# Kernel optimization log

Hardware: AMD Instinct MI355X
Metric: run time of the kernel (lower is better)

Reference implementation:

```python
import jax, jax.numpy as jnp
import numpy as np

B, N, D = 8, 1024, 256
H = 8
DH = D // H
R = 4          # relation types 0..3; adj value 4 = no relation
FF = 1024
EPS = 1e-5


def _lin(k, fan_in, shape):
    return jax.random.normal(k, shape, jnp.float32) * (1.0 / np.sqrt(fan_in))


def setup_inputs() -> dict:
    key = jax.random.key(0)
    ks = jax.random.split(key, 16)
    src = jax.random.normal(ks[0], (B, N, D), jnp.float32)
    adj_matrix = jax.random.randint(ks[1], (B, N, N), 0, 5, dtype=jnp.int32)
    Wq = _lin(ks[2], D, (D, D)); bq = jnp.zeros((D,), jnp.float32)
    Wk = _lin(ks[3], D, (D, D)); bk = jnp.zeros((D,), jnp.float32)
    Wv = _lin(ks[4], D, (R, D, D)); bv = jnp.zeros((R, D), jnp.float32)
    Wo = _lin(ks[5], D, (D, D)); bo = jnp.zeros((D,), jnp.float32)
    W1 = _lin(ks[6], D, (D, FF)); b1 = jnp.zeros((FF,), jnp.float32)
    W2 = _lin(ks[7], FF, (FF, D)); b2 = jnp.zeros((D,), jnp.float32)
    g1 = jnp.ones((D,), jnp.float32); beta1 = jnp.zeros((D,), jnp.float32)
    g2 = jnp.ones((D,), jnp.float32); beta2 = jnp.zeros((D,), jnp.float32)
    return dict(src=src, adj_matrix=adj_matrix, Wq=Wq, bq=bq, Wk=Wk, bk=bk,
                Wv=Wv, bv=bv, Wo=Wo, bo=bo, W1=W1, b1=b1, W2=W2, b2=b2,
                g1=g1, beta1=beta1, g2=g2, beta2=beta2)


def _ln(x, g, b):
    m = x.mean(-1, keepdims=True)
    v = ((x - m) ** 2).mean(-1, keepdims=True)
    return (x - m) * jax.lax.rsqrt(v + EPS) * g + b


def reference(src, adj_matrix, Wq, bq, Wk, bk, Wv, bv, Wo, bo, W1, b1, W2, b2, g1, beta1, g2, beta2):
    Bb, Nn, Dm = src.shape
    h, dh = H, Dm // H
    q = (src @ Wq + bq).reshape(Bb, Nn, h, dh).transpose(0, 2, 1, 3)  # (B,H,N,dh)
    k = (src @ Wk + bk).reshape(Bb, Nn, h, dh).transpose(0, 2, 1, 3)
    scores = jnp.einsum('bhid,bhjd->bhij', q, k) / np.sqrt(dh)
    attn = jax.nn.softmax(scores, axis=-1)                             # (B,H,N,N)
    out = jnp.zeros_like(q)
    for r in range(Wv.shape[0]):  # small fixed relation loop, matches module
        v_r = (src @ Wv[r] + bv[r]).reshape(Bb, Nn, h, dh).transpose(0, 2, 1, 3)
        mask = (adj_matrix == r)[:, None]                              # (B,1,N,N)
        out = out + jnp.einsum('bhij,bhjd->bhid', attn * mask, v_r)
    attn_out = out.transpose(0, 2, 1, 3).reshape(Bb, Nn, Dm) @ Wo + bo
    x = _ln(src + attn_out, g1, beta1)
    ff = jax.nn.gelu(x @ W1 + b1, approximate=False) @ W2 + b2
    return _ln(x + ff, g2, beta2)
```

## Files before the change

kernel.cpp:

```cpp
#include <hip/hip_runtime.h>
#include <hip/hip_bf16.h>
#include <cmath>

constexpr int CB  = 8;
constexpr int CN  = 1024;
constexpr int CD  = 256;
constexpr int CH  = 8;
constexpr int CDH = 32;
constexpr int CR  = 4;
constexpr int CFF = 1024;
constexpr float CEPS = 1e-5f;
constexpr float CS = 0.25503480f;
constexpr size_t SZH = (size_t)CB * CH * CN * CDH;

#define MODE_QK    0
#define MODE_FFN1  2
#define MODE_VT    4

typedef float v4f __attribute__((ext_vector_type(4)));
typedef short v8s __attribute__((ext_vector_type(8)));

static __device__ __forceinline__ short f2bf(float f) {
    unsigned u = __builtin_bit_cast(unsigned, f);
    u += 0x7fff + ((u >> 16) & 1);
    return (short)(u >> 16);
}
static __device__ __forceinline__ float bf2f(short s) {
    unsigned u = ((unsigned)(unsigned short)s) << 16;
    return __builtin_bit_cast(float, u);
}
static __device__ __forceinline__ unsigned cvtpk_bf16(float lo, float hi) {
    unsigned r;
    asm("v_cvt_pk_bf16_f32 %0, %1, %2" : "=v"(r) : "v"(lo), "v"(hi));
    return r;
}

static __device__ __forceinline__ void async_copy16(const void* g, void* l) {
    __builtin_amdgcn_global_load_lds(
        (const __attribute__((address_space(1))) void*)g,
        (__attribute__((address_space(3))) void*)l, 16, 0, 0);
}

template<int BM, int BN, int MODE>
__device__ __forceinline__ void gemm_body(
    const short* __restrict__ A, const short* __restrict__ Bw,
    const float* __restrict__ biasv, void* __restrict__ dest,
    int M, int K, int Nw, int bx, int by, short* smem)
{
    constexpr int WTM = BM / 2, WTN = BN / 2;
    constexpr int TM = WTM / 16, TN = WTN / 16;
    short* As = smem;
    short* Bs = smem + 2 * BM * 32;

    const int t    = threadIdx.x;
    const int lane = t & 63;
    const int w    = t >> 6;
    const int quad = lane >> 4, l15 = lane & 15;
    const int wm = w >> 1, wn = w & 1;
    const int m0 = bx * BM, n0 = by * BN;

    const int srow = lane >> 2;
    const int scol = (lane & 3) * 8;

    v4f acc[TM][TN];
    #pragma unroll
    for (int i = 0; i < TM; ++i)
        #pragma unroll
        for (int j = 0; j < TN; ++j) acc[i][j] = (v4f){0.f, 0.f, 0.f, 0.f};

    const int NK = K >> 5;

    auto stage = [&](int buf, int kt) {
        #pragma unroll
        for (int u = 0; u < BM / 64; ++u) {
            const int e0 = (w * (BM / 64) + u) * 512;
            const int row = (e0 >> 5) + srow;
            async_copy16(A + (size_t)(m0 + row) * K + kt + scol,
                         &As[buf * BM * 32 + e0]);
        }
        #pragma unroll
        for (int u = 0; u < BN / 64; ++u) {
            const int e0 = (w * (BN / 64) + u) * 512;
            const int row = (e0 >> 5) + srow;
            async_copy16(Bw + (size_t)(n0 + row) * K + kt + scol,
                         &Bs[buf * BN * 32 + e0]);
        }
    };

    stage(0, 0);

    for (int it = 0; it < NK; ++it) {
        __syncthreads();
        if (it + 1 < NK) stage((it + 1) & 1, (it + 1) << 5);

        const int buf = it & 1;
        v8s af[TM], bfr[TN];
        #pragma unroll
        for (int i = 0; i < TM; ++i)
            af[i] = *(const v8s*)&As[buf * BM * 32 +
                                     (wm * WTM + i * 16 + l15) * 32 + quad * 8];
        #pragma unroll
        for (int j = 0; j < TN; ++j)
            bfr[j] = *(const v8s*)&Bs[buf * BN * 32 +
                                      (wn * WTN + j * 16 + l15) * 32 + quad * 8];
        #pragma unroll
        for (int i = 0; i < TM; ++i)
            #pragma unroll
            for (int j = 0; j < TN; ++j)
                acc[i][j] = __builtin_amdgcn_mfma_f32_16x16x32_bf16(
                    af[i], bfr[j], acc[i][j], 0, 0, 0);
    }

    #pragma unroll
    for (int i = 0; i < TM; ++i) {
        #pragma unroll
        for (int j = 0; j < TN; ++j) {
            const int mb = m0 + wm * WTM + i * 16 + quad * 4;
            const int n  = n0 + wn * WTN + j * 16 + l15;
            float vals[4];
            if (MODE == MODE_VT) {
                #pragma unroll
                for (int rr = 0; rr < 4; ++rr) vals[rr] = acc[i][j][rr] + biasv[mb + rr];
            } else {
                #pragma unroll
                for (int rr = 0; rr < 4; ++rr) vals[rr] = acc[i][j][rr] + biasv[n];
            }

            if (MODE == MODE_QK) {
                if (n0 < 256) {
                    #pragma unroll
                    for (int rr = 0; rr < 4; ++rr) vals[rr] *= CS;
                }
                const int b = mb >> 10, ii0 = mb & 1023;
                const int plane = n >> 8, nn = n & 255;
                const int h = nn >> 5, d = nn & 31;
                #pragma unroll
                for (int rr = 0; rr < 4; ++rr)
                    ((short*)dest)[(size_t)plane * SZH +
                        (((size_t)(b * CH + h)) * CN + ii0 + rr) * CDH + d] =
                        f2bf(vals[rr]);
            } else if (MODE == MODE_VT) {
                const int b = n >> 10, ii = n & 1023;
                const int iip = (ii & ~63) | ((ii & 15) << 2) | ((ii >> 4) & 3);
                #pragma unroll
                for (int rr = 0; rr < 4; ++rr) {
                    const int m = mb + rr;
                    const int r2 = m >> 8, hd = m & 255;
                    const int h = hd >> 5, d = hd & 31;
                    ((short*)dest)[2 * SZH +
                        (((size_t)(r2 * 64 + b * CH + h)) * CDH + d) * CN + iip] =
                        f2bf(vals[rr]);
                }
            } else {
                #pragma unroll
                for (int rr = 0; rr < 4; ++rr) {
                    const size_t idx = (size_t)(mb + rr) * Nw + n;
                    const float xx = vals[rr];
                    const float E = exp2f(2.302217f * (xx + 0.044715f * xx * xx * xx));
                    ((short*)dest)[idx] = f2bf(xx * E / (E + 1.f));
                }
            }
        }
    }
}

template<int BM, int BN, int MODE>
__global__ __launch_bounds__(256)
void gemm_mfma(const short* __restrict__ A, const short* __restrict__ Bw,
               const float* __restrict__ biasv, void* __restrict__ dest,
               int M, int K, int Nw)
{
    extern __shared__ short smem[];
    gemm_body<BM, BN, MODE>(A, Bw, biasv, dest, M, K, Nw,
                            blockIdx.x, blockIdx.y, smem);
}

__global__ __launch_bounds__(256)
void proj_kernel(const short* __restrict__ src_bf, const short* __restrict__ wqkvT,
                 const float* __restrict__ bpack, short* __restrict__ qkv,
                 const int* __restrict__ adj, unsigned char* __restrict__ adj4)
{
    extern __shared__ short smem[];
    const int g = blockIdx.x;
    if (g < 512) {
        gemm_body<64, 128, MODE_QK>(src_bf, wqkvT, bpack, qkv,
                                    8192, 256, 512, g >> 2, g & 3, smem);
    } else if (g < 1536) {
        const int h2 = g - 512;
        gemm_body<64, 128, MODE_VT>(wqkvT + 512 * 256, src_bf, bpack + 512,
                                    qkv, 1024, 256, 8192, h2 & 15, h2 >> 4, smem);
    } else {
        const int nout = CB * CN * CN / 8;
        for (int i = (g - 1536) * 256 + threadIdx.x; i < nout; i += 512 * 256) {
            const int m   = i & 7;
            const int T   = (i >> 3) & 15;
            const int row = i >> 7;
            const int* p = adj + (size_t)row * CN + T * 64 + 2 * m;
            const int2 q0 = *(const int2*)(p);
            const int2 q1 = *(const int2*)(p + 16);
            const int2 q2 = *(const int2*)(p + 32);
            const int2 q3 = *(const int2*)(p + 48);
            const unsigned pk =
                (unsigned)(q0.x & 0xf)         | ((unsigned)(q1.x & 0xf) << 4)  |
                ((unsigned)(q2.x & 0xf) << 8)  | ((unsigned)(q3.x & 0xf) << 12) |
                ((unsigned)(q0.y & 0xf) << 16) | ((unsigned)(q1.y & 0xf) << 20) |
                ((unsigned)(q2.y & 0xf) << 24) | ((unsigned)(q3.y & 0xf) << 28);
            ((unsigned*)adj4)[i] = pk;
        }
    }
}

template<bool OUTF, bool OUTB, bool ADDBF>
__global__ __launch_bounds__(256)
void gemm_ln32(const short* __restrict__ A, const short* __restrict__ Bw,
               const float* __restrict__ biasv, const void* __restrict__ addp,
               const float* __restrict__ gw, const float* __restrict__ be,
               float* __restrict__ outf, short* __restrict__ outb, int K)
{
    __shared__ short As[2][16 * 32];
    __shared__ short Bs[2][256 * 32];
    __shared__ float redS[16][4], redQ[16][4];

    const int t    = threadIdx.x;
    const int lane = t & 63;
    const int w    = t >> 6;
    const int quad = lane >> 4, l15 = lane & 15;
    const int m0   = blockIdx.x * 16;

    const int srow = lane >> 2;
    const int scol = (lane & 3) * 8;

    v4f acc[4];
    #pragma unroll
    for (int j = 0; j < 4; ++j) acc[j] = (v4f){0.f, 0.f, 0.f, 0.f};

    const int NK = K >> 5;

    auto stage = [&](int buf, int kt) {
        if (t < 64)
            async_copy16(A + (size_t)(m0 + (t >> 2)) * K + kt + (t & 3) * 8,
                         &As[buf][t * 8]);
        #pragma unroll
        for (int u = 0; u < 4; ++u) {
            const int e0 = (w * 4 + u) * 512;
            async_copy16(Bw + (size_t)((e0 >> 5) + srow) * K + kt + scol,
                         &Bs[buf][e0]);
        }
    };

    stage(0, 0);

    for (int it = 0; it < NK; ++it) {
        __syncthreads();
        if (it + 1 < NK) stage((it + 1) & 1, (it + 1) << 5);

        const int buf = it & 1;
        const v8s af = *(const v8s*)&As[buf][l15 * 32 + quad * 8];
        #pragma unroll
        for (int j = 0; j < 4; ++j) {
            const v8s bfr = *(const v8s*)&Bs[buf][(w * 64 + 16 * j + l15) * 32 + quad * 8];
            acc[j] = __builtin_amdgcn_mfma_f32_16x16x32_bf16(af, bfr, acc[j], 0, 0, 0);
        }
    }

    float v[4][4];
    #pragma unroll
    for (int rr = 0; rr < 4; ++rr) {
        const int row = m0 + quad * 4 + rr;
        float s = 0.f, sq = 0.f;
        #pragma unroll
        for (int j = 0; j < 4; ++j) {
            const int n = w * 64 + 16 * j + l15;
            const size_t idx = (size_t)row * CD + n;
            const float addv = ADDBF ? bf2f(((const short*)addp)[idx])
                                     : ((const float*)addp)[idx];
            const float x = acc[j][rr] + biasv[n] + addv;
            v[rr][j] = x;
            s += x; sq += x * x;
        }
        #pragma unroll
        for (int off = 1; off < 16; off <<= 1) {
            s  += __shfl_xor(s, off);
            sq += __shfl_xor(sq, off);
        }
        if (l15 == 0) {
            redS[quad * 4 + rr][w] = s;
            redQ[quad * 4 + rr][w] = sq;
        }
    }
    __syncthreads();

    #pragma unroll
    for (int rr = 0; rr < 4; ++rr) {
        const int r16 = quad * 4 + rr;
        const int row = m0 + r16;
        const float s  = (redS[r16][0] + redS[r16][1]) + (redS[r16][2] + redS[r16][3]);
        const float sq = (redQ[r16][0] + redQ[r16][1]) + (redQ[r16][2] + redQ[r16][3]);
        const float mean = s * (1.f / CD);
        const float var  = sq * (1.f / CD) - mean * mean;
        const float rstd = rsqrtf(var + CEPS);
        #pragma unroll
        for (int j = 0; j < 4; ++j) {
            const int n = w * 64 + 16 * j + l15;
            const float y = (v[rr][j] - mean) * rstd * gw[n] + be[n];
            if (OUTF) outf[(size_t)row * CD + n] = y;
            if (OUTB) outb[(size_t)row * CD + n] = f2bf(y);
        }
    }
}

__global__ __launch_bounds__(256)
void prep(const float* __restrict__ src,
          const float* __restrict__ Wq, const float* __restrict__ Wk,
          const float* __restrict__ Wv, const float* __restrict__ Wo,
          const float* __restrict__ W1, const float* __restrict__ W2,
          const float* __restrict__ bq, const float* __restrict__ bk,
          const float* __restrict__ bv, const float* __restrict__ bo,
          const float* __restrict__ b1, const float* __restrict__ b2,
          short* __restrict__ src_bf,
          short* __restrict__ wqkvT, short* __restrict__ woT,
          short* __restrict__ w1T, short* __restrict__ w2T,
          float* __restrict__ bpack)
{
    __shared__ float tile[64][65];
    const int bx = blockIdx.x, t = threadIdx.x;
    if (bx < 2048) {
        const int i = bx * 256 + t;
        const float4 v = ((const float4*)src)[i];
        short4 o;
        o.x = f2bf(v.x); o.y = f2bf(v.y); o.z = f2bf(v.z); o.w = f2bf(v.w);
        ((short4*)src_bf)[i] = o;
    } else if (bx < 2288) {
        const int tt = bx - 2048;
        const float* S; short* D;
        int Sstride, Dstride, k0, srccol, dstrow;
        if (tt < 96) {
            const int tk = tt & 3, tn = tt >> 2;
            const int ng = tn * 64;
            Sstride = 256; Dstride = 256; k0 = tk * 64;
            dstrow = tn * 64; D = wqkvT;
            if (ng < 256)      { S = Wq; srccol = ng; }
            else if (ng < 512) { S = Wk; srccol = ng - 256; }
            else { const int r = (ng - 512) >> 8;
                   S = Wv + (size_t)r * 65536; srccol = (ng - 512) & 255; }
        } else if (tt < 112) {
            const int u = tt - 96, tk = u & 3, tn = u >> 2;
            S = Wo; Sstride = 256; D = woT; Dstride = 256;
            k0 = tk * 64; srccol = tn * 64; dstrow = tn * 64;
        } else if (tt < 176) {
            const int u = tt - 112, tk = u & 3, tn = u >> 2;
            S = W1; Sstride = 1024; D = w1T; Dstride = 256;
            k0 = tk * 64; srccol = tn * 64; dstrow = tn * 64;
        } else {
            const int u = tt - 176, tk = u & 15, tn = u >> 4;
            S = W2; Sstride = 256; D = w2T; Dstride = 1024;
            k0 = tk * 64; srccol = tn * 64; dstrow = tn * 64;
        }
        #pragma unroll
        for (int u2 = 0; u2 < 4; ++u2) {
            const int kl = (t >> 4) + u2 * 16;
            const int nl = (t & 15) * 4;
            const float4 v = *(const float4*)&S[(size_t)(k0 + kl) * Sstride + srccol + nl];
            tile[kl][nl + 0] = v.x; tile[kl][nl + 1] = v.y;
            tile[kl][nl + 2] = v.z; tile[kl][nl + 3] = v.w;
        }
        __syncthreads();
        #pragma unroll
        for (int u2 = 0; u2 < 4; ++u2) {
            const int nl = (t >> 4) + u2 * 16;
            const int kl = (t & 15) * 4;
            short4 o;
            o.x = f2bf(tile[kl + 0][nl]); o.y = f2bf(tile[kl + 1][nl]);
            o.z = f2bf(tile[kl + 2][nl]); o.w = f2bf(tile[kl + 3][nl]);
            *(short4*)&D[(size_t)(dstrow + nl) * Dstride + k0 + kl] = o;
        }
    } else {
        const int idx = (bx - 2288) * 256 + t;
        float bvv;
        if (idx < 256)       bvv = bq[idx];
        else if (idx < 512)  bvv = bk[idx - 256];
        else if (idx < 1536) bvv = bv[idx - 512];
        else if (idx < 1792) bvv = bo[idx - 1536];
        else if (idx < 2816) bvv = b1[idx - 1792];
        else                 bvv = b2[idx - 2816];
        bpack[idx] = bvv;
    }
}

__global__ __launch_bounds__(256)
void attn_mfma(const short* __restrict__ qg, const short* __restrict__ kg,
               const short* __restrict__ vt, const unsigned char* __restrict__ adj4,
               short* __restrict__ outh)
{
    __shared__ __align__(16) short ks[2][64 * 32];
    __shared__ __align__(16) short vtile[4][32][72];
    __shared__ __align__(16) short ps[64][68];
    __shared__ __align__(16) unsigned char adjs[64][40];

    const int t    = threadIdx.x;
    const int lane = t & 63;
    const int w    = t >> 6;
    const int quad = lane >> 4;
    const int l15  = lane & 15;
    const int g    = blockIdx.x;
    const int b    = g & 7;
    const int h    = (g >> 3) & 7;
    const int i0   = (g >> 6) * 64;
    const int bhh  = b * CH + h;
    const size_t bh = (size_t)bhh;

    const v8s qfrag = *(const v8s*)&qg[(bh * CN + i0 + 16 * w + l15) * CDH + quad * 8];

    v4f oacc[2];
    oacc[0] = (v4f){0.f, 0.f, 0.f, 0.f};
    oacc[1] = (v4f){0.f, 0.f, 0.f, 0.f};
    float plsum[4] = {0.f, 0.f, 0.f, 0.f};

    const int arow = 16 * w + l15;

    const int srow = lane >> 2;
    const int scol = (lane & 3) * 8;
    const int vd0  = lane >> 3;
    const int vc   = (lane & 7) * 8;
    const short* vplane = vt + (((size_t)(w * 64 + bhh)) * CDH) * CN;
    const unsigned char* adjg =
        adj4 + ((size_t)(b * CN) + i0 + (t >> 2)) * (CN / 2) + (t & 3) * 8;

    v8s vpre[4];
    int2 apre;

    async_copy16(kg + (bh * CN + 16 * w + srow) * CDH + scol,
                 &ks[0][(16 * w + srow) * 32]);
    #pragma unroll
    for (int it = 0; it < 4; ++it)
        vpre[it] = *(const v8s*)&vplane[(size_t)(vd0 + 8 * it) * CN + vc];
    apre = *(const int2*)adjg;

    for (int jt = 0; jt < 16; ++jt) {
        __syncthreads();

        #pragma unroll
        for (int it = 0; it < 4; ++it)
            *(v8s*)&vtile[w][vd0 + 8 * it][vc] = vpre[it];
        *(int2*)&adjs[t >> 2][(t & 3) * 8] = apre;
        __syncthreads();

        if (jt + 1 < 16) {
            const int j1 = (jt + 1) * 64;
            async_copy16(kg + (bh * CN + j1 + 16 * w + srow) * CDH + scol,
                         &ks[(jt + 1) & 1][(16 * w + srow) * 32]);
            #pragma unroll
            for (int it = 0; it < 4; ++it)
                vpre[it] = *(const v8s*)&vplane[(size_t)(vd0 + 8 * it) * CN + j1 + vc];
            apre = *(const int2*)(adjg + (jt + 1) * 32);
        }

        const short* ksb = ks[jt & 1];
        v4f sacc[4];
        #pragma unroll
        for (int jb = 0; jb < 4; ++jb) {
            const v8s kfrag = *(const v8s*)&ksb[(16 * jb + l15) * 32 + quad * 8];
            sacc[jb] = __builtin_amdgcn_mfma_f32_16x16x32_bf16(
                qfrag, kfrag, (v4f){0.f, 0.f, 0.f, 0.f}, 0, 0, 0);
        }

        #pragma unroll
        for (int rr = 0; rr < 4; ++rr) {
            const int prow = 16 * w + quad * 4 + rr;
            float p[4];
            #pragma unroll
            for (int jb = 0; jb < 4; ++jb) p[jb] = exp2f(sacc[jb][rr]);
            plsum[rr] += (p[0] + p[1]) + (p[2] + p[3]);
            const unsigned lo = cvtpk_bf16(p[0], p[1]);
            const unsigned hi = cvtpk_bf16(p[2], p[3]);
            *(uint2*)&ps[prow][4 * l15] = make_uint2(lo, hi);
        }

        #pragma unroll
        for (int kb = 0; kb < 2; ++kb) {
            const int4 praw = *(const int4*)&ps[arow][32 * kb + quad * 8];
            const unsigned ab32 = *(const unsigned*)&adjs[arow][16 * kb + quad * 4];
            const unsigned P[4] = {(unsigned)praw.x, (unsigned)praw.y,
                                   (unsigned)praw.z, (unsigned)praw.w};
            unsigned pf[4][4];
            #pragma unroll
            for (int u = 0; u < 4; ++u) {
                const unsigned sel = 0x0c000c00u | (unsigned)u | ((unsigned)u << 16);
                const unsigned a2 = __builtin_amdgcn_perm(ab32, ab32, sel) & 0x00F0000Fu;
                #pragma unroll
                for (int r = 0; r < 4; ++r) {
                    const unsigned x = a2 ^ ((unsigned)r | ((unsigned)r << 20));
                    unsigned tt, mm;
                    asm("v_pk_add_i16 %0, %1, %2"
                        : "=v"(tt) : "v"(x), "v"(0xffffffffu));
                    asm("v_pk_ashrrev_i16 %0, %1, %2"
                        : "=v"(mm) : "v"(0x000f000fu), "v"(tt));
                    pf[r][u] = P[u] & mm;
                }
            }
            #pragma unroll
            for (int r = 0; r < 4; ++r) {
                const v8s pfr = __builtin_bit_cast(v8s,
                    make_uint4(pf[r][0], pf[r][1], pf[r][2], pf[r][3]));
                #pragma unroll
                for (int cb = 0; cb < 2; ++cb) {
                    const v8s vfrag = *(const v8s*)&vtile[r][16 * cb + l15][32 * kb + quad * 8];
                    oacc[cb] = __builtin_amdgcn_mfma_f32_16x16x32_bf16(
                        pfr, vfrag, oacc[cb], 0, 0, 0);
                }
            }
        }
    }

    #pragma unroll
    for (int rr = 0; rr < 4; ++rr) {
        float l = plsum[rr];
        #pragma unroll
        for (int off = 1; off < 16; off <<= 1) l += __shfl_xor(l, off);
        const float inv = 1.f / l;
        const int row = i0 + 16 * w + quad * 4 + rr;
        #pragma unroll
        for (int cb = 0; cb < 2; ++cb)
            outh[((size_t)b * CN + row) * CD + h * CDH + 16 * cb + l15] =
                f2bf(oacc[cb][rr] * inv);
    }
}

extern "C" void kernel_launch(void* const* d_in, const int* in_sizes, int n_in,
                              void* d_out, int out_size, void* d_ws, size_t ws_size,
                              hipStream_t stream)
{
    const float* src = (const float*)d_in[0];
    const int*   adj = (const int*)d_in[1];
    const float* Wq  = (const float*)d_in[2];
    const float* bq  = (const float*)d_in[3];
    const float* Wk  = (const float*)d_in[4];
    const float* bk  = (const float*)d_in[5];
    const float* Wv  = (const float*)d_in[6];
    const float* bv  = (const float*)d_in[7];
    const float* Wo  = (const float*)d_in[8];
    const float* bo  = (const float*)d_in[9];
    const float* W1  = (const float*)d_in[10];
    const float* b1  = (const float*)d_in[11];
    const float* W2  = (const float*)d_in[12];
    const float* b2  = (const float*)d_in[13];
    const float* g1  = (const float*)d_in[14];
    const float* be1 = (const float*)d_in[15];
    const float* g2  = (const float*)d_in[16];
    const float* be2 = (const float*)d_in[17];
    float* out = (float*)d_out;

    char* wsb = (char*)d_ws;
    const size_t MB = (size_t)1 << 20;

    unsigned char* adj4 = (unsigned char*)(wsb);
    short* qkv_bf = (short*)(wsb + 8 * MB);
    short* src_bf = (short*)(wsb + 32 * MB);
    short* wqkvT  = (short*)(wsb + 36 * MB);
    short* woT    = (short*)(wsb + 36 * MB + 768 * 1024);
    short* w1T    = (short*)(wsb + 36 * MB + 896 * 1024);
    short* w2T    = (short*)(wsb + 36 * MB + 1408 * 1024);
    float* bpack  = (float*)(wsb + 36 * MB + 1920 * 1024);
    short* heads_bf = (short*)(wsb + 38 * MB);
    short* x_bf   = (short*)(wsb + 32 * MB);
    short* h1_bf  = (short*)(wsb + 16 * MB);

    const int M = CB * CN;
    dim3 blk(256);

    prep<<<dim3(2300), blk, 0, stream>>>(src, Wq, Wk, Wv, Wo, W1, W2,
        bq, bk, bv, bo, b1, b2, src_bf, wqkvT, woT, w1T, w2T, bpack);

    proj_kernel<<<dim3(2048), blk, 24576, stream>>>(
        src_bf, wqkvT, bpack, qkv_bf, adj, adj4);

    attn_mfma<<<dim3(1024), blk, 0, stream>>>(
        qkv_bf, qkv_bf + SZH, qkv_bf + 2 * SZH, adj4, heads_bf);

    gemm_ln32<false, true, false><<<dim3(M / 16), blk, 0, stream>>>(
        heads_bf, woT, bpack + 1536, src, g1, be1, nullptr, x_bf, CD);

    gemm_mfma<64, 128, MODE_FFN1><<<dim3(M / 64, CFF / 128), blk, 24576, stream>>>(
        x_bf, w1T, bpack + 1792, h1_bf, M, CD, CFF);

    gemm_ln32<true, false, true><<<dim3(M / 16), blk, 0, stream>>>(
        h1_bf, w2T, bpack + 2816, x_bf, g2, be2, out, nullptr, CFF);
}
```

Measured before the change: 230.3 us.

## Restructure attention tile pipeline: async V double-buffer, register K/adj prefetch, XOR swizzle

The attention kernel now loads K fragments and adjacency bytes straight into registers one tile ahead, dropping their shared-memory staging. V tiles are double-buffered in LDS through async copies that write an XOR-swizzled layout, and the P tile uses the same swizzle. This takes one __syncthreads per tile and the register-to-LDS copy off the critical path and is meant to avoid LDS bank conflicts. launch_bounds now asks for 4 blocks per SM, which may cap registers and cause spills. The prefetch on the last iteration wraps around and reloads tile 0, which is redundant work.

```diff
diff --git a/kernel.cpp b/kernel.cpp
--- a/kernel.cpp
+++ b/kernel.cpp
@@ -387,15 +387,13 @@
     }
 }
 
-__global__ __launch_bounds__(256)
+__global__ __launch_bounds__(256, 4)
 void attn_mfma(const short* __restrict__ qg, const short* __restrict__ kg,
                const short* __restrict__ vt, const unsigned char* __restrict__ adj4,
                short* __restrict__ outh)
 {
-    __shared__ __align__(16) short ks[2][64 * 32];
-    __shared__ __align__(16) short vtile[4][32][72];
-    __shared__ __align__(16) short ps[64][68];
-    __shared__ __align__(16) unsigned char adjs[64][40];
+    __shared__ __align__(16) short vtl[2][8192];
+    __shared__ __align__(16) short ps[4096];
 
     const int t    = threadIdx.x;
     const int lane = t & 63;
@@ -411,75 +409,72 @@
 
     const v8s qfrag = *(const v8s*)&qg[(bh * CN + i0 + 16 * w + l15) * CDH + quad * 8];
 
+    const short* vsrc[4];
+    #pragma unroll
+    for (int u = 0; u < 4; ++u) {
+        const int gl = t + 256 * u;
+        const int r = gl >> 8, d = (gl >> 3) & 31, gc = gl & 7;
+        vsrc[u] = vt + ((size_t)(r * 64 + bhh) * CDH + d) * CN + (gc ^ (d & 7)) * 8;
+    }
+    const short* kbase = kg + (bh * CN + l15) * CDH + quad * 8;
+    const unsigned char* abase =
+        adj4 + ((size_t)(b * CN) + i0 + 16 * w + l15) * (CN / 2) + quad * 4;
+
     v4f oacc[2];
     oacc[0] = (v4f){0.f, 0.f, 0.f, 0.f};
     oacc[1] = (v4f){0.f, 0.f, 0.f, 0.f};
     float plsum[4] = {0.f, 0.f, 0.f, 0.f};
-
     const int arow = 16 * w + l15;
-
-    const int srow = lane >> 2;
-    const int scol = (lane & 3) * 8;
-    const int vd0  = lane >> 3;
-    const int vc   = (lane & 7) * 8;
-    const short* vplane = vt + (((size_t)(w * 64 + bhh)) * CDH) * CN;
-    const unsigned char* adjg =
-        adj4 + ((size_t)(b * CN) + i0 + (t >> 2)) * (CN / 2) + (t & 3) * 8;
-
-    v8s vpre[4];
-    int2 apre;
-
-    async_copy16(kg + (bh * CN + 16 * w + srow) * CDH + scol,
-                 &ks[0][(16 * w + srow) * 32]);
-    #pragma unroll
-    for (int it = 0; it < 4; ++it)
-        vpre[it] = *(const v8s*)&vplane[(size_t)(vd0 + 8 * it) * CN + vc];
-    apre = *(const int2*)adjg;
+    const int psw  = (l15 & 7) * 8;
+
+    #pragma unroll
+    for (int u = 0; u < 4; ++u)
+        async_copy16(vsrc[u], &vtl[0][(t + 256 * u) * 8]);
+    v8s kpre[4];
+    #pragma unroll
+    for (int jb = 0; jb < 4; ++jb)
+        kpre[jb] = *(const v8s*)(kbase + (16 * jb) * CDH);
+    unsigned apre0 = *(const unsigned*)(abase);
+    unsigned apre1 = *(const unsigned*)(abase + 16);
 
     for (int jt = 0; jt < 16; ++jt) {
         __syncthreads();
-
-        #pragma unroll
-        for (int it = 0; it < 4; ++it)
-            *(v8s*)&vtile[w][vd0 + 8 * it][vc] = vpre[it];
-        *(int2*)&adjs[t >> 2][(t & 3) * 8] = apre;
-        __syncthreads();
-
-        if (jt + 1 < 16) {
-            const int j1 = (jt + 1) * 64;
-            async_copy16(kg + (bh * CN + j1 + 16 * w + srow) * CDH + scol,
-                         &ks[(jt + 1) & 1][(16 * w + srow) * 32]);
-            #pragma unroll
-            for (int it = 0; it < 4; ++it)
-                vpre[it] = *(const v8s*)&vplane[(size_t)(vd0 + 8 * it) * CN + j1 + vc];
-            apre = *(const int2*)(adjg + (jt + 1) * 32);
-        }
-
-        const short* ksb = ks[jt & 1];
+        const int p = jt & 1;
+
         v4f sacc[4];
         #pragma unroll
-        for (int jb = 0; jb < 4; ++jb) {
-            const v8s kfrag = *(const v8s*)&ksb[(16 * jb + l15) * 32 + quad * 8];
+        for (int jb = 0; jb < 4; ++jb)
             sacc[jb] = __builtin_amdgcn_mfma_f32_16x16x32_bf16(
-                qfrag, kfrag, (v4f){0.f, 0.f, 0.f, 0.f}, 0, 0, 0);
-        }
+                qfrag, kpre[jb], (v4f){0.f, 0.f, 0.f, 0.f}, 0, 0, 0);
+
+        const unsigned a0 = apre0, a1 = apre1;
+        const int jn = (jt + 1) & 15;
+        #pragma unroll
+        for (int u = 0; u < 4; ++u)
+            async_copy16(vsrc[u] + jn * 64, &vtl[p ^ 1][(t + 256 * u) * 8]);
+        #pragma unroll
+        for (int jb = 0; jb < 4; ++jb)
+            kpre[jb] = *(const v8s*)(kbase + (jn * 64 + 16 * jb) * CDH);
+        apre0 = *(const unsigned*)(abase + jn * 32);
+        apre1 = *(const unsigned*)(abase + jn * 32 + 16);
 
         #pragma unroll
         for (int rr = 0; rr < 4; ++rr) {
             const int prow = 16 * w + quad * 4 + rr;
-            float p[4];
+            float pv[4];
             #pragma unroll
-            for (int jb = 0; jb < 4; ++jb) p[jb] = exp2f(sacc[jb][rr]);
-            plsum[rr] += (p[0] + p[1]) + (p[2] + p[3]);
-            const unsigned lo = cvtpk_bf16(p[0], p[1]);
-            const unsigned hi = cvtpk_bf16(p[2], p[3]);
-            *(uint2*)&ps[prow][4 * l15] = make_uint2(lo, hi);
+            for (int jb = 0; jb < 4; ++jb) pv[jb] = exp2f(sacc[jb][rr]);
+            plsum[rr] += (pv[0] + pv[1]) + (pv[2] + pv[3]);
+            const unsigned lo = cvtpk_bf16(pv[0], pv[1]);
+            const unsigned hi = cvtpk_bf16(pv[2], pv[3]);
+            const int off = prow * 64 + (((l15 >> 1) ^ (prow & 7)) * 8) + (l15 & 1) * 4;
+            *(uint2*)&ps[off] = make_uint2(lo, hi);
         }
 
         #pragma unroll
         for (int kb = 0; kb < 2; ++kb) {
-            const int4 praw = *(const int4*)&ps[arow][32 * kb + quad * 8];
-            const unsigned ab32 = *(const unsigned*)&adjs[arow][16 * kb + quad * 4];
+            const int4 praw = *(const int4*)&ps[arow * 64 + (((4 * kb + quad) * 8) ^ psw)];
+            const unsigned ab32 = kb ? a1 : a0;
             const unsigned P[4] = {(unsigned)praw.x, (unsigned)praw.y,
                                    (unsigned)praw.z, (unsigned)praw.w};
             unsigned pf[4][4];
@@ -504,7 +499,8 @@
                     make_uint4(pf[r][0], pf[r][1], pf[r][2], pf[r][3]));
                 #pragma unroll
                 for (int cb = 0; cb < 2; ++cb) {
-                    const v8s vfrag = *(const v8s*)&vtile[r][16 * cb + l15][32 * kb + quad * 8];
+                    const v8s vfrag = *(const v8s*)&vtl[p][r * 2048 +
+                        (16 * cb + l15) * 64 + (((4 * kb + quad) * 8) ^ psw)];
                     oacc[cb] = __builtin_amdgcn_mfma_f32_16x16x32_bf16(
                         pfr, vfrag, oacc[cb], 0, 0, 0);
                 }
```

Result: no change. 229.0 us (-0.6%).
